# Performance work log

Hardware: AMD Instinct MI355X
Metric: run time of the kernel (lower is better)

The kernel has to match this reference:

```python
import jax, jax.numpy as jnp
import numpy as np

D = 1024      # input_dim
E = 8         # num_experts
H = 4096      # expert_hidden
O = 1024      # expert_out
K = 2         # top_k
N = 8192      # tokens


def setup_inputs() -> dict:
    key = jax.random.key(0)
    ks = jax.random.split(key, 10)
    s = lambda fan_in: 1.0 / np.sqrt(fan_in)
    return {
        "x": jax.random.normal(ks[0], (N, D), dtype=jnp.float32),
        # expert params, stacked over E
        "W1": jax.random.uniform(ks[1], (E, D, H), jnp.float32, -s(D), s(D)),
        "b1": jnp.zeros((E, H), jnp.float32),
        "W2": jax.random.uniform(ks[2], (E, H, O), jnp.float32, -s(H), s(H)),
        "b2": jnp.zeros((E, O), jnp.float32),
        # gate MLP: D -> 4D -> D -> E
        "G1": jax.random.uniform(ks[3], (D, 4 * D), jnp.float32, -s(D), s(D)),
        "g1": jnp.zeros((4 * D,), jnp.float32),
        "G2": jax.random.uniform(ks[4], (4 * D, D), jnp.float32, -s(4 * D), s(4 * D)),
        "g2": jnp.zeros((D,), jnp.float32),
        "G3": jax.random.uniform(ks[5], (D, E), jnp.float32, -s(D), s(D)),
        "g3": jnp.zeros((E,), jnp.float32),
    }


def reference(x, W1, b1, W2, b2, G1, g1, G2, g2, G3, g3):
    # gate logits: 3-layer MLP with ReLUs
    h = jax.nn.relu(x @ G1 + g1)
    h = jax.nn.relu(h @ G2 + g2)
    gate_logits = h @ G3 + g3                      # [N, E]

    # top-k routing: softmax over selected logits, scattered to dense [N, E]
    topv, topi = jax.lax.top_k(gate_logits, K)     # [N, K]
    top_p = jax.nn.softmax(topv, axis=1)
    rows = jnp.arange(x.shape[0])[:, None]
    p = jnp.zeros_like(gate_logits).at[rows, topi].set(top_p)  # [N, E]

    # dense all-experts MLP (faithful to torch.stack over all experts)
    hid = jax.nn.relu(jnp.einsum('nd,edh->enh', x, W1) + b1[:, None, :])  # [E, N, H]
    out = jnp.einsum('enh,eho->eno', hid, W2) + b2[:, None, :]            # [E, N, O]

    # gate-weighted combine
    y = jnp.einsum('ne,eno->no', p, out)           # [N, O]
    return (y, p)
```

## Files before the change

### kernel.cpp

```cpp
#include <hip/hip_runtime.h>
#include <stdint.h>

#define N_ 8192
#define D_ 1024
#define E_ 8
#define H_ 4096
#define O_ 1024

using f16 = _Float16;
using f16x8 = __attribute__((ext_vector_type(8))) _Float16;
using f32x4 = __attribute__((ext_vector_type(4))) float;

__device__ __forceinline__ f32x4 mfma16(f16x8 a, f16x8 b, f32x4 c) {
  return __builtin_amdgcn_mfma_f32_16x16x32_f16(a, b, c, 0, 0, 0);
}

__device__ __forceinline__ int imin(int a, int b) { return a < b ? a : b; }

__global__ void splitx_k(const float* __restrict__ in, f16* __restrict__ oh,
                         f16* __restrict__ ol, int n) {
  int i = blockIdx.x * blockDim.x + threadIdx.x;
  if (i >= n) return;
  float v = in[i];
  f16 h = (f16)v;
  oh[i] = h;
  ol[i] = (f16)((v - (float)h) * 2048.0f);
}

template <bool SPLIT>
__global__ void tcast_k(const float* __restrict__ in, f16* __restrict__ oh,
                        f16* __restrict__ ol, int R, int C) {
  __shared__ float tile[32][33];
  const int b = blockIdx.z;
  const float* inb = in + (size_t)b * R * C;
  f16* ohb = oh + (size_t)b * R * C;
  f16* olb = SPLIT ? (ol + (size_t)b * R * C) : nullptr;
  const int c0 = blockIdx.x * 32, r0 = blockIdx.y * 32;
  const int tx = threadIdx.x, ty = threadIdx.y;
#pragma unroll
  for (int j = 0; j < 4; j++)
    tile[ty + 8 * j][tx] = inb[(size_t)(r0 + ty + 8 * j) * C + (c0 + tx)];
  __syncthreads();
#pragma unroll
  for (int j = 0; j < 4; j++) {
    float v = tile[tx][ty + 8 * j];
    f16 h = (f16)v;
    size_t oi = (size_t)(c0 + ty + 8 * j) * R + (r0 + tx);
    ohb[oi] = h;
    if constexpr (SPLIT) olb[oi] = (f16)((v - (float)h) * 2048.0f);
  }
}

template <bool SPLIT, int MODE, int OUT>
__global__ __launch_bounds__(256, 2) void gemm_k(
    const f16* __restrict__ Ah, const f16* __restrict__ Al,
    const f16* __restrict__ Bh, const f16* __restrict__ Bl, size_t Bstride,
    const float* __restrict__ bias, int biasStride,
    void* __restrict__ out0, void* __restrict__ out1,
    int M, int N, int K,
    const int* __restrict__ cnt, const int* __restrict__ offs,
    const int* __restrict__ rowid) {
  const uint32_t nwg = gridDim.x * gridDim.y * gridDim.z;
  uint32_t hwid = blockIdx.x + gridDim.x * (blockIdx.y + gridDim.y * blockIdx.z);
  uint32_t lg = ((nwg & 7) == 0) ? ((hwid & 7) * (nwg >> 3) + (hwid >> 3)) : hwid;
  const int bX = lg % gridDim.x;
  const uint32_t lg2 = lg / gridDim.x;
  const int bY = lg2 % gridDim.y;
  const int bZ = lg2 / gridDim.y;

  const int z = bZ;
  const int rows = (MODE == 0) ? M : cnt[z];
  const int rowBase = bX * 128;
  if (rowBase >= rows) return;
  const int colBase = bY * 128;
  const int tid = threadIdx.x, wave = tid >> 6, lane = tid & 63;

  constexpr int NT = SPLIT ? 4 : 2;
  __shared__ __align__(16) f16 lds[2 * NT * 8192];

  const f16* BhZ = Bh + (size_t)z * Bstride;
  const f16* BlZ = SPLIT ? (Bl + (size_t)z * Bstride) : nullptr;

  const int tile_id = SPLIT ? wave : (wave >> 1);
  constexpr int NI = SPLIT ? 16 : 8;
  const int rowHalf = SPLIT ? 0 : (wave & 1) * 64;
  const bool isA = tile_id < (SPLIT ? 2 : 1);

  const int lrow = lane >> 3;
  const int kc_l = (lane & 7) ^ lrow;

  uint32_t rb[NI];
  const f16* src;
  if (isA) {
    src = (SPLIT && tile_id == 1) ? Al : Ah;
#pragma unroll
    for (int i = 0; i < NI; ++i) {
      const int ml = rowHalf + i * 8 + lrow;
      uint32_t gr;
      if (MODE == 0) {
        gr = (uint32_t)(rowBase + ml);
      } else {
        int l0 = imin(rowBase + ml, rows - 1);
        gr = (MODE == 1) ? (uint32_t)rowid[offs[z] + l0]
                         : (uint32_t)(offs[z] + l0);
      }
      rb[i] = gr * (uint32_t)K;
    }
  } else {
    src = (SPLIT && tile_id == 3) ? BlZ : BhZ;
#pragma unroll
    for (int i = 0; i < NI; ++i) {
      const int ml = rowHalf + i * 8 + lrow;
      rb[i] = (uint32_t)(colBase + ml) * (uint32_t)K;
    }
  }

  f32x4 acc[4][4] = {};
  f32x4 acc2[SPLIT ? 4 : 1][SPLIT ? 4 : 1] = {};

  const int wr = wave >> 1, wc = wave & 1, lm = lane & 15, q4 = lane >> 4;
  const int swA = lm & 7;

  const int stageOff = tile_id * 8192 + rowHalf * 64;

  auto stage = [&](int b, int kt) {
    f16* dst = lds + b * (NT * 8192) + stageOff;
#pragma unroll
    for (int i = 0; i < NI; ++i) {
      const f16* g = src + (size_t)rb[i] + (size_t)kt + kc_l * 8;
      __builtin_amdgcn_global_load_lds(
          (const __attribute__((address_space(1))) void*)g,
          (__attribute__((address_space(3))) void*)(dst + i * 512), 16, 0, 0);
    }
  };

  const int nkt = K >> 6;
  int buf = 0;
  stage(0, 0);
  __syncthreads();

  for (int t = 0; t < nkt; ++t) {
    if (t + 1 < nkt) stage(buf ^ 1, (t + 1) << 6);

    const f16* base = lds + buf * (NT * 8192);
    const f16* tA = base;
    const f16* tAl = base + 8192;
    const f16* tB = base + (SPLIT ? 2 : 1) * 8192;
    const f16* tBl = base + 3 * 8192;

#pragma unroll
    for (int s = 0; s < 2; ++s) {
      const int kc = s * 4 + q4;
      const int sw = (kc ^ swA) * 8;
      f16x8 a_h[4], b_h[4];
      f16x8 a_l[SPLIT ? 4 : 1], b_l[SPLIT ? 4 : 1];
#pragma unroll
      for (int i = 0; i < 4; i++) {
        int m = wr * 64 + i * 16 + lm;
        a_h[i] = *(const f16x8*)(tA + (size_t)m * 64 + sw);
        if constexpr (SPLIT)
          a_l[i] = *(const f16x8*)(tAl + (size_t)m * 64 + sw);
      }
#pragma unroll
      for (int j = 0; j < 4; j++) {
        int n = wc * 64 + j * 16 + lm;
        b_h[j] = *(const f16x8*)(tB + (size_t)n * 64 + sw);
        if constexpr (SPLIT)
          b_l[j] = *(const f16x8*)(tBl + (size_t)n * 64 + sw);
      }
#pragma unroll
      for (int i = 0; i < 4; i++)
#pragma unroll
        for (int j = 0; j < 4; j++) {
          acc[i][j] = mfma16(a_h[i], b_h[j], acc[i][j]);
          if constexpr (SPLIT) {
            acc2[i][j] = mfma16(a_h[i], b_l[j], acc2[i][j]);
            acc2[i][j] = mfma16(a_l[i], b_h[j], acc2[i][j]);
          }
        }
    }
    __syncthreads();
    buf ^= 1;
  }

  if constexpr (OUT == 0 || OUT == 2) {
    float* lb = (float*)lds;
#pragma unroll
    for (int j = 0; j < 4; j++) {
      const int n = wc * 64 + j * 16 + lm;
      const float bb = bias[(size_t)z * biasStride + colBase + n];
#pragma unroll
      for (int i = 0; i < 4; i++) {
#pragma unroll
        for (int t = 0; t < 4; t++) {
          const int r = wr * 64 + i * 16 + q4 * 4 + t;
          float v = acc[i][j][t];
          if constexpr (SPLIT) v += acc2[i][j][t] * (1.0f / 2048.0f);
          v = fmaxf(v + bb, 0.0f);
          lb[r * 128 + n] = v;
        }
      }
    }
    __syncthreads();
#pragma unroll
    for (int it = 0; it < 8; ++it) {
      const int r = it * 16 + (tid >> 4);
      const int c = (tid & 15) * 8;
      const float* p = lb + r * 128 + c;
      f16x8 hv, lv;
#pragma unroll
      for (int e = 0; e < 8; e++) {
        float v = p[e];
        f16 h = (f16)v;
        hv[e] = h;
        if constexpr (OUT == 0) lv[e] = (f16)((v - (float)h) * 2048.0f);
      }
      if constexpr (OUT == 0) {
        *(f16x8*)((f16*)out0 + (size_t)(rowBase + r) * N + colBase + c) = hv;
        *(f16x8*)((f16*)out1 + (size_t)(rowBase + r) * N + colBase + c) = lv;
      } else {
        if (rowBase + r < rows)
          *(f16x8*)((f16*)out0 +
                    ((size_t)offs[z] + rowBase + r) * N + colBase + c) = hv;
      }
    }
  } else {
#pragma unroll
    for (int j = 0; j < 4; j++) {
      const int n = colBase + wc * 64 + j * 16 + lm;
      const float bb = bias[(size_t)z * biasStride + n];
#pragma unroll
      for (int i = 0; i < 4; i++) {
#pragma unroll
        for (int t = 0; t < 4; t++) {
          const int lr = rowBase + wr * 64 + i * 16 + q4 * 4 + t;
          float v = acc[i][j][t];
          if constexpr (SPLIT) v += acc2[i][j][t] * (1.0f / 2048.0f);
          v += bb;
          if constexpr (OUT == 1) {
            v = fmaxf(v, 0.0f);
            ((float*)out0)[(size_t)lr * N + n] = v;
          } else {
            if (lr < rows) {
              ((float*)out0)[((size_t)offs[z] + lr) * N + n] = v;
            }
          }
        }
      }
    }
  }
}

__global__ void logits_k(const float* __restrict__ h2, const float* __restrict__ G3,
                         const float* __restrict__ g3, float* __restrict__ logits) {
  const int t = blockIdx.x * 4 + (threadIdx.x >> 6);
  const int lane = threadIdx.x & 63;
  float acc[8] = {};
  const float* row = h2 + (size_t)t * 1024;
  for (int k = lane; k < 1024; k += 64) {
    float hv = row[k];
    const float* g = G3 + (size_t)k * 8;
#pragma unroll
    for (int e = 0; e < 8; e++) acc[e] += hv * g[e];
  }
#pragma unroll
  for (int e = 0; e < 8; e++) {
    float v = acc[e];
    for (int o = 32; o; o >>= 1) v += __shfl_down(v, o);
    if (lane == 0) logits[(size_t)t * 8 + e] = v + g3[e];
  }
}

__global__ void top2_k(const float* __restrict__ logits, float* __restrict__ pdense,
                       int* __restrict__ ti, float* __restrict__ tp,
                       int* __restrict__ cnt) {
  int t = blockIdx.x * blockDim.x + threadIdx.x;
  if (t >= N_) return;
  float v1 = -1e30f, v2 = -1e30f;
  int i1 = 0, i2 = 0;
#pragma unroll
  for (int e = 0; e < 8; e++) {
    float v = logits[(size_t)t * 8 + e];
    if (v > v1) { v2 = v1; i2 = i1; v1 = v; i1 = e; }
    else if (v > v2) { v2 = v; i2 = e; }
  }
  float e2 = expf(v2 - v1);
  float inv = 1.0f / (1.0f + e2);
  float p1 = inv, p2 = e2 * inv;
#pragma unroll
  for (int e = 0; e < 8; e++)
    pdense[(size_t)t * 8 + e] = (e == i1) ? p1 : ((e == i2) ? p2 : 0.0f);
  ti[2 * t] = i1; ti[2 * t + 1] = i2;
  tp[2 * t] = p1; tp[2 * t + 1] = p2;
  atomicAdd(&cnt[i1], 1);
  atomicAdd(&cnt[i2], 1);
}

__global__ void prefix_k(const int* __restrict__ cnt, int* __restrict__ offs,
                         int* __restrict__ cur) {
  if (threadIdx.x == 0 && blockIdx.x == 0) {
    int s = 0;
    for (int e = 0; e < E_; e++) { offs[e] = s; cur[e] = s; s += cnt[e]; }
    offs[E_] = s;
  }
}

__global__ void place_k(const int* __restrict__ ti, int* __restrict__ cur,
                        int* __restrict__ rowid, int* __restrict__ slotof) {
  int t = blockIdx.x * blockDim.x + threadIdx.x;
  if (t >= N_) return;
#pragma unroll
  for (int k = 0; k < 2; k++) {
    int e = ti[2 * t + k];
    int slot = atomicAdd(&cur[e], 1);
    rowid[slot] = t;
    slotof[2 * t + k] = slot;
  }
}

__global__ void combine_k(const float* __restrict__ out_slots,
                          const int* __restrict__ slotof,
                          const float* __restrict__ tp, float* __restrict__ y) {
  const int t = blockIdx.x;
  const int c = threadIdx.x * 4;
  const int s0 = slotof[2 * t], s1 = slotof[2 * t + 1];
  const float p0 = tp[2 * t], p1 = tp[2 * t + 1];
  const float4 a = *(const float4*)(out_slots + (size_t)s0 * O_ + c);
  const float4 b = *(const float4*)(out_slots + (size_t)s1 * O_ + c);
  float4 r;
  r.x = p0 * a.x + p1 * b.x;
  r.y = p0 * a.y + p1 * b.y;
  r.z = p0 * a.z + p1 * b.z;
  r.w = p0 * a.w + p1 * b.w;
  *(float4*)(y + (size_t)t * O_ + c) = r;
}

extern "C" void kernel_launch(void* const* d_in, const int* in_sizes, int n_in,
                              void* d_out, int out_size, void* d_ws, size_t ws_size,
                              hipStream_t stream) {
  const float* x  = (const float*)d_in[0];
  const float* W1 = (const float*)d_in[1];
  const float* b1 = (const float*)d_in[2];
  const float* W2 = (const float*)d_in[3];
  const float* b2 = (const float*)d_in[4];
  const float* G1 = (const float*)d_in[5];
  const float* g1 = (const float*)d_in[6];
  const float* G2 = (const float*)d_in[7];
  const float* g2 = (const float*)d_in[8];
  const float* G3 = (const float*)d_in[9];
  const float* g3 = (const float*)d_in[10];

  float* y = (float*)d_out;
  float* pdense = y + (size_t)N_ * O_;

  char* w = (char*)d_ws;
  auto alloc = [&](size_t bytes) -> char* {
    char* p = w;
    w += (bytes + 255) & ~(size_t)255;
    return p;
  };
  f16* xh  = (f16*)alloc((size_t)N_ * D_ * 2);
  f16* xl  = (f16*)alloc((size_t)N_ * D_ * 2);
  f16* G1h = (f16*)alloc((size_t)D_ * H_ * 2);
  f16* G1l = (f16*)alloc((size_t)D_ * H_ * 2);
  f16* G2h = (f16*)alloc((size_t)H_ * D_ * 2);
  f16* G2l = (f16*)alloc((size_t)H_ * D_ * 2);
  f16* W1t = (f16*)alloc((size_t)E_ * D_ * H_ * 2);
  f16* W2t = (f16*)alloc((size_t)E_ * H_ * O_ * 2);
  f16* h1h = (f16*)alloc((size_t)N_ * H_ * 2);
  f16* h1l = (f16*)alloc((size_t)N_ * H_ * 2);
  float* h2 = (float*)alloc((size_t)N_ * D_ * 4);
  float* logits = (float*)alloc((size_t)N_ * E_ * 4);
  int*   ti  = (int*)alloc((size_t)N_ * 2 * 4);
  float* tp  = (float*)alloc((size_t)N_ * 2 * 4);
  int*   cnt = (int*)alloc(64);
  int*   cur = (int*)alloc(64);
  int*   offs = (int*)alloc(64);
  int*   rowid = (int*)alloc((size_t)N_ * 2 * 4);
  int*   slotof = (int*)alloc((size_t)N_ * 2 * 4);
  f16*   hid = (f16*)alloc((size_t)N_ * 2 * H_ * 2);

  float* out_slots = (float*)h1h;

  hipMemsetAsync(cnt, 0, 64, stream);

  splitx_k<<<(N_ * D_) / 256, 256, 0, stream>>>(x, xh, xl, N_ * D_);
  tcast_k<true><<<dim3(H_ / 32, D_ / 32, 1), dim3(32, 8), 0, stream>>>(G1, G1h, G1l, D_, H_);
  tcast_k<true><<<dim3(D_ / 32, H_ / 32, 1), dim3(32, 8), 0, stream>>>(G2, G2h, G2l, H_, D_);
  tcast_k<false><<<dim3(H_ / 32, D_ / 32, E_), dim3(32, 8), 0, stream>>>(W1, W1t, nullptr, D_, H_);
  tcast_k<false><<<dim3(O_ / 32, H_ / 32, E_), dim3(32, 8), 0, stream>>>(W2, W2t, nullptr, H_, O_);

  gemm_k<true, 0, 0><<<dim3(64, 32, 1), 256, 0, stream>>>(
      xh, xl, G1h, G1l, 0, g1, 0, h1h, h1l, N_, H_, D_,
      nullptr, nullptr, nullptr);
  gemm_k<true, 0, 1><<<dim3(64, 8, 1), 256, 0, stream>>>(
      h1h, h1l, G2h, G2l, 0, g2, 0, h2, nullptr, N_, D_, H_,
      nullptr, nullptr, nullptr);
  logits_k<<<N_ / 4, 256, 0, stream>>>(h2, G3, g3, logits);

  top2_k<<<N_ / 256, 256, 0, stream>>>(logits, pdense, ti, tp, cnt);
  prefix_k<<<1, 64, 0, stream>>>(cnt, offs, cur);
  place_k<<<N_ / 256, 256, 0, stream>>>(ti, cur, rowid, slotof);

  gemm_k<false, 1, 2><<<dim3(64, 32, E_), 256, 0, stream>>>(
      xh, nullptr, W1t, nullptr, (size_t)D_ * H_, b1, H_, hid, nullptr,
      N_, H_, D_, cnt, offs, rowid);
  gemm_k<false, 2, 3><<<dim3(64, 8, E_), 256, 0, stream>>>(
      hid, nullptr, W2t, nullptr, (size_t)H_ * O_, b2, O_, out_slots, nullptr,
      N_, O_, H_, cnt, offs, rowid);

  combine_k<<<N_, 256, 0, stream>>>(out_slots, slotof, tp, y);
}
```

Before: 1.887 ms.

## Single-buffer GEMM LDS to raise occupancy and swizzle epilogue staging

Removes double-buffered LDS staging so each workgroup uses half the shared memory, and raises launch bounds from 2 to 4 workgroups per CU. The epilogue writes its fp32 tile through LDS in two half passes with an XOR swizzle and vectorized float4 reads, so the smaller buffer is enough. In exchange, global-to-LDS loads no longer overlap with MFMA compute inside a workgroup and an extra barrier is added per k-step. Latency hiding now has to come from more resident waves, and the tighter register budget may cause spills, especially for the split-precision variant.

```diff
diff --git a/kernel.cpp b/kernel.cpp
--- a/kernel.cpp
+++ b/kernel.cpp
@@ -52,7 +52,7 @@
 }
 
 template <bool SPLIT, int MODE, int OUT>
-__global__ __launch_bounds__(256, 2) void gemm_k(
+__global__ __launch_bounds__(256, 4) void gemm_k(
     const f16* __restrict__ Ah, const f16* __restrict__ Al,
     const f16* __restrict__ Bh, const f16* __restrict__ Bl, size_t Bstride,
     const float* __restrict__ bias, int biasStride,
@@ -76,7 +76,7 @@
   const int tid = threadIdx.x, wave = tid >> 6, lane = tid & 63;
 
   constexpr int NT = SPLIT ? 4 : 2;
-  __shared__ __align__(16) f16 lds[2 * NT * 8192];
+  __shared__ __align__(16) f16 lds[NT * 8192];
 
   const f16* BhZ = Bh + (size_t)z * Bstride;
   const f16* BlZ = SPLIT ? (Bl + (size_t)z * Bstride) : nullptr;
@@ -120,34 +120,23 @@
 
   const int wr = wave >> 1, wc = wave & 1, lm = lane & 15, q4 = lane >> 4;
   const int swA = lm & 7;
-
-  const int stageOff = tile_id * 8192 + rowHalf * 64;
-
-  auto stage = [&](int b, int kt) {
-    f16* dst = lds + b * (NT * 8192) + stageOff;
+  const f16* tA = lds;
+  const f16* tAl = lds + 8192;
+  const f16* tB = lds + (SPLIT ? 2 : 1) * 8192;
+  const f16* tBl = lds + 3 * 8192;
+
+  f16* dstBase = lds + (size_t)tile_id * 8192 + (size_t)rowHalf * 64;
+
+  for (int kt = 0; kt < K; kt += 64) {
+    if (kt) __syncthreads();
 #pragma unroll
     for (int i = 0; i < NI; ++i) {
       const f16* g = src + (size_t)rb[i] + (size_t)kt + kc_l * 8;
       __builtin_amdgcn_global_load_lds(
           (const __attribute__((address_space(1))) void*)g,
-          (__attribute__((address_space(3))) void*)(dst + i * 512), 16, 0, 0);
-    }
-  };
-
-  const int nkt = K >> 6;
-  int buf = 0;
-  stage(0, 0);
-  __syncthreads();
-
-  for (int t = 0; t < nkt; ++t) {
-    if (t + 1 < nkt) stage(buf ^ 1, (t + 1) << 6);
-
-    const f16* base = lds + buf * (NT * 8192);
-    const f16* tA = base;
-    const f16* tAl = base + 8192;
-    const f16* tB = base + (SPLIT ? 2 : 1) * 8192;
-    const f16* tBl = base + 3 * 8192;
-
+          (__attribute__((address_space(3))) void*)(dstBase + i * 512), 16, 0, 0);
+    }
+    __syncthreads();
 #pragma unroll
     for (int s = 0; s < 2; ++s) {
       const int kc = s * 4 + q4;
@@ -179,50 +168,62 @@
           }
         }
     }
+  }
+
+  if constexpr (OUT == 0 || OUT == 2) {
     __syncthreads();
-    buf ^= 1;
-  }
-
-  if constexpr (OUT == 0 || OUT == 2) {
     float* lb = (float*)lds;
 #pragma unroll
-    for (int j = 0; j < 4; j++) {
-      const int n = wc * 64 + j * 16 + lm;
-      const float bb = bias[(size_t)z * biasStride + colBase + n];
-#pragma unroll
-      for (int i = 0; i < 4; i++) {
-#pragma unroll
-        for (int t = 0; t < 4; t++) {
-          const int r = wr * 64 + i * 16 + q4 * 4 + t;
-          float v = acc[i][j][t];
-          if constexpr (SPLIT) v += acc2[i][j][t] * (1.0f / 2048.0f);
-          v = fmaxf(v + bb, 0.0f);
-          lb[r * 128 + n] = v;
+    for (int pass = 0; pass < 2; ++pass) {
+      if (wr == pass) {
+#pragma unroll
+        for (int j = 0; j < 4; j++) {
+          const int n = wc * 64 + j * 16 + lm;
+          const float bb = bias[(size_t)z * biasStride + colBase + n];
+#pragma unroll
+          for (int i = 0; i < 4; i++) {
+#pragma unroll
+            for (int t = 0; t < 4; t++) {
+              const int r = i * 16 + q4 * 4 + t;
+              float v = acc[i][j][t];
+              if constexpr (SPLIT) v += acc2[i][j][t] * (1.0f / 2048.0f);
+              v = fmaxf(v + bb, 0.0f);
+              lb[r * 128 + (n ^ ((r & 7) << 2))] = v;
+            }
+          }
         }
       }
-    }
-    __syncthreads();
-#pragma unroll
-    for (int it = 0; it < 8; ++it) {
-      const int r = it * 16 + (tid >> 4);
-      const int c = (tid & 15) * 8;
-      const float* p = lb + r * 128 + c;
-      f16x8 hv, lv;
-#pragma unroll
-      for (int e = 0; e < 8; e++) {
-        float v = p[e];
-        f16 h = (f16)v;
-        hv[e] = h;
-        if constexpr (OUT == 0) lv[e] = (f16)((v - (float)h) * 2048.0f);
-      }
-      if constexpr (OUT == 0) {
-        *(f16x8*)((f16*)out0 + (size_t)(rowBase + r) * N + colBase + c) = hv;
-        *(f16x8*)((f16*)out1 + (size_t)(rowBase + r) * N + colBase + c) = lv;
-      } else {
-        if (rowBase + r < rows)
-          *(f16x8*)((f16*)out0 +
-                    ((size_t)offs[z] + rowBase + r) * N + colBase + c) = hv;
-      }
+      __syncthreads();
+      {
+        const int rr = tid >> 4;
+        const int cc = (tid & 15) * 8;
+#pragma unroll
+        for (int it = 0; it < 4; ++it) {
+          const int r = it * 16 + rr;
+          const int X = (r & 7) << 2;
+          const float4 v0 = *(const float4*)(lb + r * 128 + (cc ^ X));
+          const float4 v1 = *(const float4*)(lb + r * 128 + ((cc + 4) ^ X));
+          const float vv[8] = {v0.x, v0.y, v0.z, v0.w, v1.x, v1.y, v1.z, v1.w};
+          f16x8 hv, lv;
+#pragma unroll
+          for (int e = 0; e < 8; e++) {
+            float v = vv[e];
+            f16 h = (f16)v;
+            hv[e] = h;
+            if constexpr (OUT == 0) lv[e] = (f16)((v - (float)h) * 2048.0f);
+          }
+          const int gr = rowBase + pass * 64 + r;
+          if constexpr (OUT == 0) {
+            *(f16x8*)((f16*)out0 + (size_t)gr * N + colBase + cc) = hv;
+            *(f16x8*)((f16*)out1 + (size_t)gr * N + colBase + cc) = lv;
+          } else {
+            if (gr < rows)
+              *(f16x8*)((f16*)out0 +
+                        ((size_t)offs[z] + gr) * N + colBase + cc) = hv;
+          }
+        }
+      }
+      __syncthreads();
     }
   } else {
 #pragma unroll
```

After: 1.911 ms. No clear change (+1.3%).
